# Performance work log

Hardware: AMD Instinct MI355X
Metric: run time of the kernel (lower is better)

Reference implementation:

```python
import jax, jax.numpy as jnp
import numpy as np

DIM = 1024
HEADS = 16
DIM_HEAD = 64
INNER = HEADS * DIM_HEAD  # 1024
EPS = 1e-5


def setup_inputs() -> dict:
    key = jax.random.key(0)
    ks = jax.random.split(key, 8)
    B, N = 4, 2048
    s = 0.02
    return {
        "query": jax.random.normal(ks[0], (B, N, DIM), jnp.float32),
        "key_": jax.random.normal(ks[1], (B, N, DIM), jnp.float32),
        "value": jax.random.normal(ks[2], (B, N, DIM), jnp.float32),
        "Wq": jax.random.normal(ks[3], (DIM, INNER), jnp.float32) * s,
        "Wk": jax.random.normal(ks[4], (DIM, INNER), jnp.float32) * s,
        "Wv": jax.random.normal(ks[5], (DIM, INNER), jnp.float32) * s,
        "Wo": jax.random.normal(ks[6], (INNER, DIM), jnp.float32) * s,
        "bo": jnp.zeros((DIM,), jnp.float32),
        "gamma": jnp.ones((DIM,), jnp.float32),
        "beta": jnp.zeros((DIM,), jnp.float32),
    }


def reference(query, key_, value, Wq, Wk, Wv, Wo, bo, gamma, beta):
    B, N, _ = query.shape
    scale = DIM_HEAD ** (-0.5)
    # project and split heads: [B, H, N, Dh]
    q = (query @ Wq).reshape(B, N, HEADS, DIM_HEAD).transpose(0, 2, 1, 3)
    k = (key_ @ Wk).reshape(B, N, HEADS, DIM_HEAD).transpose(0, 2, 1, 3)
    v = (value @ Wv).reshape(B, N, HEADS, DIM_HEAD).transpose(0, 2, 1, 3)
    dots = jnp.einsum("bhnd,bhmd->bhnm", q, k) * scale  # [B,H,N,N]
    attn = jax.nn.softmax(dots, axis=-1)
    out = jnp.einsum("bhnm,bhmd->bhnd", attn, v)
    out = out.transpose(0, 2, 1, 3).reshape(B, N, INNER)
    out = out @ Wo + bo  # dropout p=0.0 is identity
    # LayerNorm over last dim
    mu = out.mean(-1, keepdims=True)
    var = ((out - mu) ** 2).mean(-1, keepdims=True)
    normed = (out - mu) * jax.lax.rsqrt(var + EPS) * gamma + beta
    return normed + query
```

## Files before the change

### kernel.cpp

```cpp
#include <hip/hip_runtime.h>
#include <stdint.h>

#define K_DIM 1024
#define B_SZ 4
#define N_SEQ 2048
#define HEADS 16
#define DH 64
#define M_TOT (B_SZ * N_SEQ)

typedef __bf16 bf16x8 __attribute__((ext_vector_type(8)));
typedef __bf16 bf16x4 __attribute__((ext_vector_type(4)));
typedef float f32x4 __attribute__((ext_vector_type(4)));
typedef float f32x8 __attribute__((ext_vector_type(8)));
typedef short s16x4 __attribute__((ext_vector_type(4)));

typedef const uint32_t __attribute__((address_space(1))) gas_u32;
typedef uint32_t __attribute__((address_space(3))) las_u32;

#define CE_SCALE 0.1803368801f

__device__ __forceinline__ uint16_t f2bf(float f) {
  uint32_t u = __float_as_uint(f);
  u += 0x7FFFu + ((u >> 16) & 1u);
  return (uint16_t)(u >> 16);
}

__device__ __forceinline__ void gld_lds16(const uint16_t* g, uint16_t* lds) {
  __builtin_amdgcn_global_load_lds((gas_u32*)g, (las_u32*)lds, 16, 0, 0);
}

#if defined(__has_builtin)
#if __has_builtin(__builtin_amdgcn_mfma_f32_16x16x16bf16_1k)
#define HAVE_MFMA16_BUILTIN 1
#endif
#endif

__device__ __forceinline__ f32x4 mfma16(bf16x4 a, bf16x4 b, f32x4 c) {
#ifdef HAVE_MFMA16_BUILTIN
  return __builtin_amdgcn_mfma_f32_16x16x16bf16_1k(
      __builtin_bit_cast(s16x4, a), __builtin_bit_cast(s16x4, b), c, 0, 0, 0);
#else
  f32x4 d;
  asm("v_mfma_f32_16x16x16_bf16 %0, %1, %2, %3"
      : "=v"(d)
      : "v"(a), "v"(b), "v"(c));
  return d;
#endif
}

__global__ __launch_bounds__(256) void transpose_conv(const float* __restrict__ s0,
                                                      const float* __restrict__ s1,
                                                      const float* __restrict__ s2,
                                                      const float* __restrict__ s3,
                                                      uint16_t* __restrict__ dstbase) {
  __shared__ float tile[32][33];
  const int z = blockIdx.z;
  const float* src = (z == 0) ? s0 : (z == 1) ? s1 : (z == 2) ? s2 : s3;
  uint16_t* dst = dstbase + (size_t)z * 1024 * 1024;
  const int tx = threadIdx.x, ty = threadIdx.y;
  const int bx = blockIdx.x * 32, by = blockIdx.y * 32;
#pragma unroll
  for (int i = 0; i < 32; i += 8)
    tile[ty + i][tx] = src[(size_t)(by + ty + i) * 1024 + bx + tx];
  __syncthreads();
#pragma unroll
  for (int i = 0; i < 32; i += 8)
    dst[(size_t)(bx + ty + i) * 1024 + by + tx] = f2bf(tile[tx][ty + i]);
}

__global__ __launch_bounds__(256, 2) void gemm_qkv(const float* __restrict__ Aq,
                                                   const float* __restrict__ Ak,
                                                   const float* __restrict__ Av,
                                                   const uint16_t* __restrict__ BT,
                                                   uint16_t* __restrict__ Cout) {
  __shared__ __align__(16) uint16_t As[128 * 32];
  __shared__ __align__(16) uint16_t Bs[128 * 32];
  const int tid = threadIdx.x;
  const int wave = tid >> 6, lane = tid & 63;
  const int g = lane >> 4, c16 = lane & 15;

  const int bid = blockIdx.x;
  const int xcd = bid & 7;
  const int l = bid >> 3;
  const int z = l >> 6;
  const int r = l & 63;
  const int n0 = (r & 7) * 128;
  const int m0 = (xcd * 8 + (r >> 3)) * 128;

  const int wr = wave >> 1, wc = wave & 1;
  const float* A = (z == 0) ? Aq : (z == 1) ? Ak : Av;
  const uint16_t* Bz = BT + (size_t)z * 1024 * 1024;
  const float scale = (z == 0) ? CE_SCALE : 1.f;

  const f32x4 fzero = {0.f, 0.f, 0.f, 0.f};
  f32x4 acc[4][4];
#pragma unroll
  for (int i = 0; i < 4; ++i)
#pragma unroll
    for (int j = 0; j < 4; ++j) acc[i][j] = fzero;

  const int srow = wave * 32 + (lane >> 2);
  const int scol = (lane & 3) * 8;
  const float* ag0 = A + (size_t)(m0 + srow) * K_DIM + scol;
  const float* ag1 = A + (size_t)(m0 + srow + 16) * K_DIM + scol;
  const uint16_t* bg0 = Bz + (size_t)(n0 + srow) * K_DIM + scol;
  const uint16_t* bg1 = Bz + (size_t)(n0 + srow + 16) * K_DIM + scol;
  uint16_t* lb0 = &Bs[(wave * 32) * 32];
  uint16_t* lb1 = &Bs[(wave * 32 + 16) * 32];
  uint16_t* la0 = &As[srow * 32 + scol];
  uint16_t* la1 = &As[(srow + 16) * 32 + scol];

  f32x4 ar0, ar1, ar2, ar3;
  ar0 = *(const f32x4*)(ag0);
  ar1 = *(const f32x4*)(ag0 + 4);
  ar2 = *(const f32x4*)(ag1);
  ar3 = *(const f32x4*)(ag1 + 4);

  for (int kt = 0; kt < K_DIM / 32; ++kt) {
    __syncthreads();
    {
      f32x8 f0 = __builtin_shufflevector(ar0, ar1, 0, 1, 2, 3, 4, 5, 6, 7);
      f32x8 f1 = __builtin_shufflevector(ar2, ar3, 0, 1, 2, 3, 4, 5, 6, 7);
      *(bf16x8*)la0 = __builtin_convertvector(f0, bf16x8);
      *(bf16x8*)la1 = __builtin_convertvector(f1, bf16x8);
    }
    gld_lds16(bg0 + kt * 32, lb0);
    gld_lds16(bg1 + kt * 32, lb1);
    __syncthreads();

    if (kt < K_DIM / 32 - 1) {
      const int ko = (kt + 1) * 32;
      ar0 = *(const f32x4*)(ag0 + ko);
      ar1 = *(const f32x4*)(ag0 + ko + 4);
      ar2 = *(const f32x4*)(ag1 + ko);
      ar3 = *(const f32x4*)(ag1 + ko + 4);
    }

    bf16x8 avec[4], bvec[4];
#pragma unroll
    for (int i = 0; i < 4; ++i)
      avec[i] = *(const bf16x8*)&As[(wr * 64 + i * 16 + c16) * 32 + g * 8];
#pragma unroll
    for (int j = 0; j < 4; ++j)
      bvec[j] = *(const bf16x8*)&Bs[(wc * 64 + j * 16 + c16) * 32 + g * 8];
#pragma unroll
    for (int i = 0; i < 4; ++i)
#pragma unroll
      for (int j = 0; j < 4; ++j)
        acc[i][j] = __builtin_amdgcn_mfma_f32_16x16x32_bf16(avec[i], bvec[j], acc[i][j], 0, 0, 0);
  }

#pragma unroll
  for (int i = 0; i < 4; ++i) {
#pragma unroll
    for (int j = 0; j < 4; ++j) {
      const int col = n0 + wc * 64 + j * 16 + c16;
      if (z == 2) {
        const int h = col >> 6, d = col & 63;
        const int row0 = m0 + wr * 64 + i * 16 + g * 4;
        const int b = row0 >> 11, n = row0 & 2047;
        ushort4 o;
        o.x = f2bf(acc[i][j][0]); o.y = f2bf(acc[i][j][1]);
        o.z = f2bf(acc[i][j][2]); o.w = f2bf(acc[i][j][3]);
        *(ushort4*)&Cout[(size_t)2 * M_TOT * 1024 +
                         (((size_t)(b * HEADS + h)) * DH + d) * N_SEQ + n] = o;
      } else {
#pragma unroll
        for (int r2 = 0; r2 < 4; ++r2) {
          const int row = m0 + wr * 64 + i * 16 + g * 4 + r2;
          const int b = row >> 11, n = row & 2047;
          const int h = col >> 6, d = col & 63;
          Cout[(size_t)z * M_TOT * 1024 + (((size_t)(b * HEADS + h)) * N_SEQ + n) * DH + d] =
              f2bf(acc[i][j][r2] * scale);
        }
      }
    }
  }
}

__global__ __launch_bounds__(256, 2) void gemm_out(const uint16_t* __restrict__ A,
                                                   const uint16_t* __restrict__ BT,
                                                   float* __restrict__ Cout,
                                                   const float* __restrict__ bias) {
  __shared__ __align__(16) uint16_t As[128 * 32];
  __shared__ __align__(16) uint16_t Bs[128 * 32];
  const int tid = threadIdx.x;
  const int wave = tid >> 6, lane = tid & 63;
  const int g = lane >> 4, c16 = lane & 15;

  const int bid = blockIdx.x;
  const int xcd = bid & 7;
  const int l = bid >> 3;
  const int n0 = (l & 7) * 128;
  const int m0 = (xcd * 8 + (l >> 3)) * 128;
  const int wr = wave >> 1, wc = wave & 1;

  const f32x4 fzero = {0.f, 0.f, 0.f, 0.f};
  f32x4 acc[4][4];
#pragma unroll
  for (int i = 0; i < 4; ++i)
#pragma unroll
    for (int j = 0; j < 4; ++j) acc[i][j] = fzero;

  const int srow = wave * 32 + (lane >> 2);
  const int scol = (lane & 3) * 8;
  const uint16_t* ag0 = A + (size_t)(m0 + srow) * K_DIM + scol;
  const uint16_t* ag1 = A + (size_t)(m0 + srow + 16) * K_DIM + scol;
  const uint16_t* bg0 = BT + (size_t)(n0 + srow) * K_DIM + scol;
  const uint16_t* bg1 = BT + (size_t)(n0 + srow + 16) * K_DIM + scol;
  uint16_t* la0 = &As[(wave * 32) * 32];
  uint16_t* la1 = &As[(wave * 32 + 16) * 32];
  uint16_t* lb0 = &Bs[(wave * 32) * 32];
  uint16_t* lb1 = &Bs[(wave * 32 + 16) * 32];

  for (int kt = 0; kt < K_DIM / 32; ++kt) {
    __syncthreads();
    gld_lds16(ag0 + kt * 32, la0);
    gld_lds16(ag1 + kt * 32, la1);
    gld_lds16(bg0 + kt * 32, lb0);
    gld_lds16(bg1 + kt * 32, lb1);
    __syncthreads();
    bf16x8 avec[4], bvec[4];
#pragma unroll
    for (int i = 0; i < 4; ++i)
      avec[i] = *(const bf16x8*)&As[(wr * 64 + i * 16 + c16) * 32 + g * 8];
#pragma unroll
    for (int j = 0; j < 4; ++j)
      bvec[j] = *(const bf16x8*)&Bs[(wc * 64 + j * 16 + c16) * 32 + g * 8];
#pragma unroll
    for (int i = 0; i < 4; ++i)
#pragma unroll
      for (int j = 0; j < 4; ++j)
        acc[i][j] = __builtin_amdgcn_mfma_f32_16x16x32_bf16(avec[i], bvec[j], acc[i][j], 0, 0, 0);
  }

#pragma unroll
  for (int i = 0; i < 4; ++i) {
#pragma unroll
    for (int j = 0; j < 4; ++j) {
      const int col = n0 + wc * 64 + j * 16 + c16;
#pragma unroll
      for (int r2 = 0; r2 < 4; ++r2) {
        const int row = m0 + wr * 64 + i * 16 + g * 4 + r2;
        Cout[(size_t)row * 1024 + col] = acc[i][j][r2] + bias[col];
      }
    }
  }
}

__global__ __launch_bounds__(256, 2) void attention_k(const uint16_t* __restrict__ qm,
                                                      const uint16_t* __restrict__ km,
                                                      const uint16_t* __restrict__ vtm,
                                                      uint16_t* __restrict__ om) {
  __shared__ __align__(16) uint16_t Ks[64 * 64];
  __shared__ __align__(16) uint16_t Vs[64 * 64];
  const int tid = threadIdx.x;
  const int wave = tid >> 6, lane = tid & 63;
  const int g = lane >> 4, c16 = lane & 15;

  const int bid = blockIdx.x;
  const int xcd = bid & 7;
  const int l0 = bid >> 3;
  const int bh = xcd * 8 + (l0 & 7);
  const int qblk = l0 >> 3;
  const int b = bh >> 4, h = bh & 15;
  const int q0 = qblk * 256 + wave * 64;

  const uint16_t* qbase = qm + (size_t)bh * N_SEQ * DH;
  const uint16_t* kbase = km + (size_t)bh * N_SEQ * DH;
  const uint16_t* vbase = vtm + (size_t)bh * DH * N_SEQ;

  bf16x8 qf[4][2];
#pragma unroll
  for (int qc = 0; qc < 4; ++qc) {
    const uint16_t* qp = qbase + (size_t)(q0 + qc * 16 + c16) * DH + g * 8;
    qf[qc][0] = *(const bf16x8*)qp;
    qf[qc][1] = *(const bf16x8*)(qp + 32);
  }

  const f32x4 fz = {0.f, 0.f, 0.f, 0.f};
  f32x4 oacc[4][4];
#pragma unroll
  for (int qc = 0; qc < 4; ++qc)
#pragma unroll
    for (int jt = 0; jt < 4; ++jt) oacc[qc][jt] = fz;
  float l[4] = {0.f, 0.f, 0.f, 0.f};

  const int sw = c16 & 7;

  const int ch = tid & 7;
  const int krow0 = tid >> 3, krow1 = (256 + tid) >> 3;
  const int kdst0 = krow0 * 64 + ((ch ^ (krow0 & 7)) << 3);
  const int kdst1 = krow1 * 64 + ((ch ^ (krow1 & 7)) << 3);

  uint4 kp0, kp1, vp0, vp1;
  kp0 = *(const uint4*)&kbase[(size_t)tid * 8];
  kp1 = *(const uint4*)&kbase[(size_t)(256 + tid) * 8];
  vp0 = *(const uint4*)&vbase[(size_t)krow0 * N_SEQ + ch * 8];
  vp1 = *(const uint4*)&vbase[(size_t)krow1 * N_SEQ + ch * 8];
  *(uint4*)&Ks[kdst0] = kp0;
  *(uint4*)&Ks[kdst1] = kp1;
  *(uint4*)&Vs[kdst0] = vp0;
  *(uint4*)&Vs[kdst1] = vp1;
  __syncthreads();

  for (int t = 0; t < N_SEQ / 64; ++t) {
    if (t < N_SEQ / 64 - 1) {
      const size_t ko = (size_t)(t + 1) * 4096;
      const int vc = (t + 1) * 64;
      kp0 = *(const uint4*)&kbase[ko + (size_t)tid * 8];
      kp1 = *(const uint4*)&kbase[ko + (size_t)(256 + tid) * 8];
      vp0 = *(const uint4*)&vbase[(size_t)krow0 * N_SEQ + vc + ch * 8];
      vp1 = *(const uint4*)&vbase[(size_t)krow1 * N_SEQ + vc + ch * 8];
    }

#pragma unroll
    for (int kt = 0; kt < 4; ++kt) {
      const int krow = kt * 16 + c16;
      bf16x8 kf0 = *(const bf16x8*)&Ks[krow * 64 + ((g ^ sw) << 3)];
      bf16x8 kf1 = *(const bf16x8*)&Ks[krow * 64 + (((4 + g) ^ sw) << 3)];
      bf16x4 pk[4];
#pragma unroll
      for (int qc = 0; qc < 4; ++qc) {
        f32x4 z = fz;
        z = __builtin_amdgcn_mfma_f32_16x16x32_bf16(kf0, qf[qc][0], z, 0, 0, 0);
        z = __builtin_amdgcn_mfma_f32_16x16x32_bf16(kf1, qf[qc][1], z, 0, 0, 0);
        f32x4 pv;
        pv[0] = __builtin_amdgcn_exp2f(z[0]);
        pv[1] = __builtin_amdgcn_exp2f(z[1]);
        pv[2] = __builtin_amdgcn_exp2f(z[2]);
        pv[3] = __builtin_amdgcn_exp2f(z[3]);
        l[qc] += (pv[0] + pv[1]) + (pv[2] + pv[3]);
        pk[qc] = __builtin_convertvector(pv, bf16x4);
      }
#pragma unroll
      for (int jt = 0; jt < 4; ++jt) {
        bf16x4 vb = *(const bf16x4*)&Vs[(jt * 16 + c16) * 64 +
                                        (((kt * 2 + (g >> 1)) ^ sw) << 3) + (g & 1) * 4];
#pragma unroll
        for (int qc = 0; qc < 4; ++qc) oacc[qc][jt] = mfma16(pk[qc], vb, oacc[qc][jt]);
      }
    }

    if (t < N_SEQ / 64 - 1) {
      __syncthreads();
      *(uint4*)&Ks[kdst0] = kp0;
      *(uint4*)&Ks[kdst1] = kp1;
      *(uint4*)&Vs[kdst0] = vp0;
      *(uint4*)&Vs[kdst1] = vp1;
      __syncthreads();
    }
  }

#pragma unroll
  for (int qc = 0; qc < 4; ++qc) {
    l[qc] += __shfl_xor(l[qc], 16);
    l[qc] += __shfl_xor(l[qc], 32);
  }

#pragma unroll
  for (int qc = 0; qc < 4; ++qc) {
#pragma unroll
    for (int r = 0; r < 4; ++r) {
      const float lr = __shfl(l[qc], g * 4 + r, 16);
      const float inv = 1.f / lr;
      const int row = q0 + qc * 16 + g * 4 + r;
      const size_t base = ((size_t)b * N_SEQ + row) * 1024 + h * 64;
#pragma unroll
      for (int jt = 0; jt < 4; ++jt)
        om[base + jt * 16 + c16] = f2bf(oacc[qc][jt][r] * inv);
    }
  }
}

__global__ __launch_bounds__(256) void ln_res_k(const float* __restrict__ proj,
                                                const float* __restrict__ query,
                                                const float* __restrict__ gamma,
                                                const float* __restrict__ beta,
                                                float* __restrict__ out) {
  const int row = blockIdx.x;
  const int tid = threadIdx.x;
  const size_t base = (size_t)row * 1024 + tid * 4;
  float4 v = *(const float4*)(proj + base);
  float s = v.x + v.y + v.z + v.w;
  float s2 = v.x * v.x + v.y * v.y + v.z * v.z + v.w * v.w;
#pragma unroll
  for (int off = 1; off < 64; off <<= 1) {
    s += __shfl_xor(s, off);
    s2 += __shfl_xor(s2, off);
  }
  __shared__ float red[8];
  const int wave = tid >> 6, lane = tid & 63;
  if (lane == 0) { red[wave] = s; red[4 + wave] = s2; }
  __syncthreads();
  s = red[0] + red[1] + red[2] + red[3];
  s2 = red[4] + red[5] + red[6] + red[7];
  const float mu = s * (1.f / 1024.f);
  const float var = fmaxf(s2 * (1.f / 1024.f) - mu * mu, 0.f);
  const float rstd = rsqrtf(var + 1e-5f);
  float4 gq = *(const float4*)(gamma + tid * 4);
  float4 bq = *(const float4*)(beta + tid * 4);
  float4 qq = *(const float4*)(query + base);
  float4 o;
  o.x = (v.x - mu) * rstd * gq.x + bq.x + qq.x;
  o.y = (v.y - mu) * rstd * gq.y + bq.y + qq.y;
  o.z = (v.z - mu) * rstd * gq.z + bq.z + qq.z;
  o.w = (v.w - mu) * rstd * gq.w + bq.w + qq.w;
  *(float4*)(out + base) = o;
}

extern "C" void kernel_launch(void* const* d_in, const int* in_sizes, int n_in,
                              void* d_out, int out_size, void* d_ws, size_t ws_size,
                              hipStream_t stream) {
  (void)in_sizes; (void)n_in; (void)out_size; (void)ws_size;
  const float* query = (const float*)d_in[0];
  const float* key_ = (const float*)d_in[1];
  const float* value = (const float*)d_in[2];
  const float* Wq = (const float*)d_in[3];
  const float* Wk = (const float*)d_in[4];
  const float* Wv = (const float*)d_in[5];
  const float* Wo = (const float*)d_in[6];
  const float* bo = (const float*)d_in[7];
  const float* gamma = (const float*)d_in[8];
  const float* beta = (const float*)d_in[9];
  float* out = (float*)d_out;

  const size_t NELEM = (size_t)M_TOT * 1024;
  uint16_t* wsp = (uint16_t*)d_ws;
  uint16_t* WqT = wsp;
  uint16_t* WoT = WqT + 3 * 1024 * 1024;
  uint16_t* qb = wsp + 4 * 1024 * 1024;
  uint16_t* attnO = qb + 3 * NELEM;
  float* proj = (float*)(attnO + NELEM);

  transpose_conv<<<dim3(32, 32, 4), dim3(32, 8), 0, stream>>>(Wq, Wk, Wv, Wo, WqT);

  gemm_qkv<<<1536, 256, 0, stream>>>(query, key_, value, WqT, qb);

  attention_k<<<512, 256, 0, stream>>>(qb, qb + NELEM, qb + 2 * NELEM, attnO);

  gemm_out<<<512, 256, 0, stream>>>(attnO, WoT, proj, bo);

  ln_res_k<<<8192, 256, 0, stream>>>(proj, query, gamma, beta, out);
}
```

Measured before the change: 367.4 us.

## Load fp32 A tiles directly to LDS via global_load_lds with XOR swizzle

The QKV GEMM no longer loads fp32 activations into registers, converts them to bf16 and writes them to LDS. It now DMAs the fp32 A tile straight into LDS with global_load_lds, using an XOR-swizzled column layout to avoid bank conflicts, and converts to bf16 when building MFMA operands. This removes register staging and the explicit LDS store. In exchange the LDS footprint for A doubles, each wave repeats the conversion work, and the register prefetch of the next tile is gone, so load latency is no longer overlapped with compute.

```diff
diff --git a/kernel.cpp b/kernel.cpp
--- a/kernel.cpp
+++ b/kernel.cpp
@@ -25,7 +25,7 @@
   return (uint16_t)(u >> 16);
 }
 
-__device__ __forceinline__ void gld_lds16(const uint16_t* g, uint16_t* lds) {
+__device__ __forceinline__ void gld_lds16(const void* g, void* lds) {
   __builtin_amdgcn_global_load_lds((gas_u32*)g, (las_u32*)lds, 16, 0, 0);
 }
 
@@ -73,7 +73,7 @@
                                                    const float* __restrict__ Av,
                                                    const uint16_t* __restrict__ BT,
                                                    uint16_t* __restrict__ Cout) {
-  __shared__ __align__(16) uint16_t As[128 * 32];
+  __shared__ __align__(16) float Asf[128 * 32];
   __shared__ __align__(16) uint16_t Bs[128 * 32];
   const int tid = threadIdx.x;
   const int wave = tid >> 6, lane = tid & 63;
@@ -99,47 +99,41 @@
 #pragma unroll
     for (int j = 0; j < 4; ++j) acc[i][j] = fzero;
 
+  const int arl = lane >> 3, ach = lane & 7;
+  const int asc = ((ach ^ (arl & 7)) << 2);
+  const float* agp[4];
+  float* adp[4];
+#pragma unroll
+  for (int q = 0; q < 4; ++q) {
+    agp[q] = A + (size_t)(m0 + wave * 32 + q * 8 + arl) * K_DIM + asc;
+    adp[q] = Asf + (wave * 32 + q * 8) * 32;
+  }
+
   const int srow = wave * 32 + (lane >> 2);
   const int scol = (lane & 3) * 8;
-  const float* ag0 = A + (size_t)(m0 + srow) * K_DIM + scol;
-  const float* ag1 = A + (size_t)(m0 + srow + 16) * K_DIM + scol;
   const uint16_t* bg0 = Bz + (size_t)(n0 + srow) * K_DIM + scol;
   const uint16_t* bg1 = Bz + (size_t)(n0 + srow + 16) * K_DIM + scol;
   uint16_t* lb0 = &Bs[(wave * 32) * 32];
   uint16_t* lb1 = &Bs[(wave * 32 + 16) * 32];
-  uint16_t* la0 = &As[srow * 32 + scol];
-  uint16_t* la1 = &As[(srow + 16) * 32 + scol];
-
-  f32x4 ar0, ar1, ar2, ar3;
-  ar0 = *(const f32x4*)(ag0);
-  ar1 = *(const f32x4*)(ag0 + 4);
-  ar2 = *(const f32x4*)(ag1);
-  ar3 = *(const f32x4*)(ag1 + 4);
 
   for (int kt = 0; kt < K_DIM / 32; ++kt) {
     __syncthreads();
-    {
-      f32x8 f0 = __builtin_shufflevector(ar0, ar1, 0, 1, 2, 3, 4, 5, 6, 7);
-      f32x8 f1 = __builtin_shufflevector(ar2, ar3, 0, 1, 2, 3, 4, 5, 6, 7);
-      *(bf16x8*)la0 = __builtin_convertvector(f0, bf16x8);
-      *(bf16x8*)la1 = __builtin_convertvector(f1, bf16x8);
-    }
+#pragma unroll
+    for (int q = 0; q < 4; ++q) gld_lds16(agp[q] + kt * 32, adp[q]);
     gld_lds16(bg0 + kt * 32, lb0);
     gld_lds16(bg1 + kt * 32, lb1);
     __syncthreads();
 
-    if (kt < K_DIM / 32 - 1) {
-      const int ko = (kt + 1) * 32;
-      ar0 = *(const f32x4*)(ag0 + ko);
-      ar1 = *(const f32x4*)(ag0 + ko + 4);
-      ar2 = *(const f32x4*)(ag1 + ko);
-      ar3 = *(const f32x4*)(ag1 + ko + 4);
-    }
-
     bf16x8 avec[4], bvec[4];
 #pragma unroll
-    for (int i = 0; i < 4; ++i)
-      avec[i] = *(const bf16x8*)&As[(wr * 64 + i * 16 + c16) * 32 + g * 8];
+    for (int i = 0; i < 4; ++i) {
+      const int rA = wr * 64 + i * 16 + c16;
+      const int rb = rA & 7;
+      f32x4 a0 = *(const f32x4*)&Asf[rA * 32 + (((2 * g) ^ rb) << 2)];
+      f32x4 a1 = *(const f32x4*)&Asf[rA * 32 + (((2 * g + 1) ^ rb) << 2)];
+      f32x8 af = __builtin_shufflevector(a0, a1, 0, 1, 2, 3, 4, 5, 6, 7);
+      avec[i] = __builtin_convertvector(af, bf16x8);
+    }
 #pragma unroll
     for (int j = 0; j < 4; ++j)
       bvec[j] = *(const bf16x8*)&Bs[(wc * 64 + j * 16 + c16) * 32 + g * 8];
```

Result: faster. 356.2 us (-3.0%).
